# Optimization experiments

Hardware: AMD Instinct MI355X
Metric: run time of the kernel (lower is better)

## Reference

```python
import jax, jax.numpy as jnp
import numpy as np

SIZE = 64

def _init_linear(key, out_f, in_f, bias):
    k1, k2 = jax.random.split(key)
    bound = 1.0 / np.sqrt(in_f)
    W = jax.random.uniform(k1, (out_f, in_f), jnp.float32, -bound, bound)
    if bias:
        b = jax.random.uniform(k2, (out_f,), jnp.float32, -bound, bound)
        return W, b
    return W, None

def setup_inputs() -> dict:
    key = jax.random.key(0)
    ks = jax.random.split(key, 8)
    B, Lq, Lc = 16, 256, 256
    query = jax.random.normal(ks[0], (B, Lq, SIZE), jnp.float32)
    bank = jax.random.normal(ks[1], (B, Lc, SIZE), jnp.float32)
    mask = jnp.zeros((B, Lq, Lc), dtype=bool)
    Wq, _ = _init_linear(ks[2], SIZE, SIZE, False)          # linear_query (no bias)
    Wc, bc = _init_linear(ks[3], SIZE, SIZE, True)           # linear_context (bias)
    Ws, bs = _init_linear(ks[4], 1, SIZE, True)              # linear_score
    Woq, _ = _init_linear(ks[5], SIZE, SIZE, False)          # linear_out_query (no bias)
    Woc, boc = _init_linear(ks[6], SIZE, SIZE, True)         # linear_out_context (bias since mlp)
    return {"query": query, "bank": bank, "mask": mask,
            "Wq": Wq, "Wc": Wc, "bc": bc, "Ws": Ws, "bs": bs,
            "Woq": Woq, "Woc": Woc, "boc": boc}

def reference(query, bank, mask, Wq, Wc, bc, Ws, bs, Woq, Woc, boc):
    # MLP (additive) attention score: tanh(Wq q + Wc c + bc) projected to scalar
    sq = jnp.einsum('bqd,ed->bqe', query, Wq)                 # [B,Lq,D]
    sc = jnp.einsum('bcd,ed->bce', bank, Wc) + bc             # [B,Lc,D]
    h = jnp.tanh(sq[:, :, None, :] + sc[:, None, :, :])       # [B,Lq,Lc,D]
    score = jnp.einsum('bqcd,od->bqc', h, Ws) + bs[0]         # [B,Lq,Lc]
    score = jnp.where(mask, -jnp.inf, score)
    attn = jax.nn.softmax(score, axis=-1)                     # [B,Lq,Lc]
    context = jnp.einsum('bqc,bcd->bqd', attn, bank)          # [B,Lq,D]
    output = (jnp.einsum('bqd,ed->bqe', context, Woc) + boc
              + jnp.einsum('bqd,ed->bqe', query, Woq))
    return (output, attn)
```

## Files before the change

kernel.cpp:

```cpp
#include <hip/hip_runtime.h>
#include <math.h>

#define B  16
#define LQ 256
#define LC 256
#define D  64
#define QT 4
#define TS   2.88539008177793f
#define L2E  1.44269504088896f
#define PAD  72
#define INPAD 36
#define TPAD 33
#define CP4  264

__global__ __launch_bounds__(256) void proj_kernel(
    const float* __restrict__ query, const float* __restrict__ bank,
    const float* __restrict__ Wq, const float* __restrict__ Wc,
    const float* __restrict__ bc,
    const float* __restrict__ Woq, const float* __restrict__ Woc,
    const float* __restrict__ boc,
    float* __restrict__ esq, float* __restrict__ esct,
    float* __restrict__ oq, float* __restrict__ wb)
{
    int t  = threadIdx.x;
    int tp = blockIdx.x >> 7;
    int rb = blockIdx.x & 127;
    int bb_x = (rb & 7) + ((rb >> 6) << 3);
    int jj   = (rb >> 3) & 7;
    int r0 = bb_x * 256 + jj * 32;

    __shared__ __align__(16) float in_t[64 * INPAD];
    __shared__ __align__(16) float w_t [64 * PAD];
    __shared__ float tr[64 * TPAD];

    const float* src = (tp & 1) ? bank : query;
    const float* W   = (tp == 0) ? Wq : (tp == 1) ? Wc : (tp == 2) ? Woq : Woc;

    #pragma unroll
    for (int it = 0; it < 2; ++it) {
        int g = it * 256 + t;
        int kc4 = g & 15, row = g >> 4;
        float4 v = *reinterpret_cast<const float4*>(src + (r0 + row) * D + kc4 * 4);
        in_t[(kc4*4+0)*INPAD + row] = v.x; in_t[(kc4*4+1)*INPAD + row] = v.y;
        in_t[(kc4*4+2)*INPAD + row] = v.z; in_t[(kc4*4+3)*INPAD + row] = v.w;
    }
    #pragma unroll
    for (int it = 0; it < 4; ++it) {
        int g = it * 256 + t;
        int kc = (g >> 8) * 4 + (g & 3);
        int row = (g >> 2) & 63;
        float4 w = *reinterpret_cast<const float4*>(W + row * D + kc * 4);
        w_t[(kc*4+0)*PAD + row] = w.x; w_t[(kc*4+1)*PAD + row] = w.y;
        w_t[(kc*4+2)*PAD + row] = w.z; w_t[(kc*4+3)*PAD + row] = w.w;
    }
    __syncthreads();

    int cg = t & 15, rg = t >> 4;
    float acc[2][4];
    #pragma unroll
    for (int i = 0; i < 2; ++i)
        #pragma unroll
        for (int j = 0; j < 4; ++j) acc[i][j] = 0.f;

    #pragma unroll 8
    for (int k = 0; k < 64; ++k) {
        float2 a2 = *reinterpret_cast<const float2*>(&in_t[k * INPAD + rg * 2]);
        float4 w4 = *reinterpret_cast<const float4*>(&w_t [k * PAD + cg * 4]);
        acc[0][0]=fmaf(a2.x,w4.x,acc[0][0]); acc[0][1]=fmaf(a2.x,w4.y,acc[0][1]);
        acc[0][2]=fmaf(a2.x,w4.z,acc[0][2]); acc[0][3]=fmaf(a2.x,w4.w,acc[0][3]);
        acc[1][0]=fmaf(a2.y,w4.x,acc[1][0]); acc[1][1]=fmaf(a2.y,w4.y,acc[1][1]);
        acc[1][2]=fmaf(a2.y,w4.z,acc[1][2]); acc[1][3]=fmaf(a2.y,w4.w,acc[1][3]);
    }

    float4 b4 = {0.f, 0.f, 0.f, 0.f};
    if (tp == 1) b4 = *reinterpret_cast<const float4*>(bc  + cg * 4);
    if (tp == 3) b4 = *reinterpret_cast<const float4*>(boc + cg * 4);

    if (tp == 1) {
        #pragma unroll
        for (int i = 0; i < 2; ++i) {
            tr[(cg*4+0)*TPAD + rg*2+i] = exp2f(TS * (acc[i][0] + b4.x));
            tr[(cg*4+1)*TPAD + rg*2+i] = exp2f(TS * (acc[i][1] + b4.y));
            tr[(cg*4+2)*TPAD + rg*2+i] = exp2f(TS * (acc[i][2] + b4.z));
            tr[(cg*4+3)*TPAD + rg*2+i] = exp2f(TS * (acc[i][3] + b4.w));
        }
        __syncthreads();
        int bb = r0 >> 8;
        int cbase = r0 & 255;
        #pragma unroll
        for (int it = 0; it < 2; ++it) {
            int g = it * 256 + t;
            int d4 = g >> 5, cl = g & 31;
            float4 o;
            o.x = tr[(4*d4+0)*TPAD + cl];
            o.y = tr[(4*d4+1)*TPAD + cl];
            o.z = tr[(4*d4+2)*TPAD + cl];
            o.w = tr[(4*d4+3)*TPAD + cl];
            *reinterpret_cast<float4*>(esct + ((bb*16 + d4)*CP4 + cbase + cl)*4) = o;
        }
    } else {
        float* dst = (tp == 0) ? esq : (tp == 2) ? oq : wb;
        #pragma unroll
        for (int i = 0; i < 2; ++i) {
            float4 o;
            o.x = acc[i][0] + b4.x; o.y = acc[i][1] + b4.y;
            o.z = acc[i][2] + b4.z; o.w = acc[i][3] + b4.w;
            if (tp == 0) {
                o.x = exp2f(TS * o.x); o.y = exp2f(TS * o.y);
                o.z = exp2f(TS * o.z); o.w = exp2f(TS * o.w);
            }
            *reinterpret_cast<float4*>(dst + (r0 + rg*2 + i) * D + cg * 4) = o;
        }
    }
}

__global__ __launch_bounds__(256, 4) void attn_kernel(
    const unsigned char* __restrict__ mask,
    const float* __restrict__ esq_g, const float* __restrict__ esct_g,
    const float* __restrict__ Ws,
    const float* __restrict__ oq_g, const float* __restrict__ wb_g,
    float* __restrict__ out, float* __restrict__ attn_out)
{
    int t = threadIdx.x;
    int c = t;
    int p = blockIdx.x;
    int b = (p & 7) + ((p >> 9) << 3);
    int qb = (p >> 3) & 63;
    int bq0 = b * LQ + qb * QT;
    int lane = t & 63, wv = t >> 6;

    __shared__ __align__(16) float a_lds[QT][LC];
    __shared__ float part_lds[4 * QT * 64];
    __shared__ float red_s[4 * QT];

    const float* eqp = esq_g + bq0 * D;

    unsigned char mb[QT];
    #pragma unroll
    for (int qi = 0; qi < QT; ++qi) mb[qi] = mask[(bq0 + qi) * LC + c];

    const float4* ep4 = reinterpret_cast<const float4*>(esct_g) + b*16*CP4 + c;

    float s[QT];
    #pragma unroll
    for (int qi = 0; qi < QT; ++qi) s[qi] = 0.f;

    #pragma unroll
    for (int kb = 0; kb < 4; ++kb) {
        float4 ec4[4];
        #pragma unroll
        for (int j = 0; j < 4; ++j) ec4[j] = ep4[(kb*4 + j) * CP4];
        #pragma unroll
        for (int j = 0; j < 4; ++j) {
            const int d0 = kb * 16 + j * 4;
            float w0 = Ws[d0+0], w1 = Ws[d0+1];
            float w2 = Ws[d0+2], w3 = Ws[d0+3];
            #pragma unroll
            for (int qi = 0; qi < QT; ++qi) {
                float e0 = eqp[qi*D + d0+0];
                float e1 = eqp[qi*D + d0+1];
                float e2 = eqp[qi*D + d0+2];
                float e3 = eqp[qi*D + d0+3];
                float ax = fmaf(ec4[j].x, e0, 1.0f);
                float ay = fmaf(ec4[j].y, e1, 1.0f);
                float az = fmaf(ec4[j].z, e2, 1.0f);
                float aw = fmaf(ec4[j].w, e3, 1.0f);
                float pxy = ax * ay, pzw = az * aw;
                float nxy = fmaf(w0, ay, w1 * ax);
                float nzw = fmaf(w2, aw, w3 * az);
                float N   = fmaf(nxy, pzw, nzw * pxy);
                s[qi] = fmaf(N, __builtin_amdgcn_rcpf(pxy * pzw), s[qi]);
            }
        }
    }

    float a[QT];
    #pragma unroll
    for (int qi = 0; qi < QT; ++qi) {
        a[qi] = mb[qi] ? 0.0f : exp2f(-TS * s[qi]);
    }

    #pragma unroll
    for (int qi = 0; qi < QT; ++qi) a_lds[qi][c] = a[qi];
    #pragma unroll
    for (int qi = 0; qi < QT; ++qi) {
        float ss = a[qi];
        #pragma unroll
        for (int o = 32; o > 0; o >>= 1) ss += __shfl_xor(ss, o);
        if (lane == 0) red_s[wv * QT + qi] = ss;
    }
    __syncthreads();

    float rs[QT];
    #pragma unroll
    for (int qi = 0; qi < QT; ++qi) {
        float SUM = (red_s[qi] + red_s[QT + qi]) + (red_s[2*QT + qi] + red_s[3*QT + qi]);
        rs[qi] = __builtin_amdgcn_rcpf(SUM);
    }

    #pragma unroll
    for (int qi = 0; qi < QT; ++qi)
        attn_out[(bq0 + qi) * LC + c] = a[qi] * rs[qi];

    {
        int g = wv;
        float acc[QT];
        #pragma unroll
        for (int qi = 0; qi < QT; ++qi) acc[qi] = 0.f;
        const float* wbp = wb_g + (b * LC + g * 64) * D + lane;
        #pragma unroll
        for (int i0 = 0; i0 < 64; i0 += 4) {
            float4 A0 = *reinterpret_cast<const float4*>(&a_lds[0][g*64 + i0]);
            float4 A1 = *reinterpret_cast<const float4*>(&a_lds[1][g*64 + i0]);
            float4 A2 = *reinterpret_cast<const float4*>(&a_lds[2][g*64 + i0]);
            float4 A3 = *reinterpret_cast<const float4*>(&a_lds[3][g*64 + i0]);
            float w0 = wbp[(i0+0) * D];
            float w1 = wbp[(i0+1) * D];
            float w2 = wbp[(i0+2) * D];
            float w3 = wbp[(i0+3) * D];
            acc[0] = fmaf(A0.x, w0, acc[0]); acc[1] = fmaf(A1.x, w0, acc[1]);
            acc[2] = fmaf(A2.x, w0, acc[2]); acc[3] = fmaf(A3.x, w0, acc[3]);
            acc[0] = fmaf(A0.y, w1, acc[0]); acc[1] = fmaf(A1.y, w1, acc[1]);
            acc[2] = fmaf(A2.y, w1, acc[2]); acc[3] = fmaf(A3.y, w1, acc[3]);
            acc[0] = fmaf(A0.z, w2, acc[0]); acc[1] = fmaf(A1.z, w2, acc[1]);
            acc[2] = fmaf(A2.z, w2, acc[2]); acc[3] = fmaf(A3.z, w2, acc[3]);
            acc[0] = fmaf(A0.w, w3, acc[0]); acc[1] = fmaf(A1.w, w3, acc[1]);
            acc[2] = fmaf(A2.w, w3, acc[2]); acc[3] = fmaf(A3.w, w3, acc[3]);
        }
        #pragma unroll
        for (int qi = 0; qi < QT; ++qi)
            part_lds[(g * QT + qi) * 64 + lane] = acc[qi];
    }
    __syncthreads();

    {
        int qi = t >> 6, e = t & 63;
        float ps = (part_lds[(0 * QT + qi) * 64 + e] + part_lds[(1 * QT + qi) * 64 + e])
                 + (part_lds[(2 * QT + qi) * 64 + e] + part_lds[(3 * QT + qi) * 64 + e]);
        out[bq0 * D + t] = fmaf(ps, rs[qi], oq_g[bq0 * D + t]);
    }
}

extern "C" void kernel_launch(void* const* d_in, const int* in_sizes, int n_in,
                              void* d_out, int out_size, void* d_ws, size_t ws_size,
                              hipStream_t stream) {
    const float* query = (const float*)d_in[0];
    const float* bank  = (const float*)d_in[1];
    const unsigned char* mask = (const unsigned char*)d_in[2];
    const float* Wq  = (const float*)d_in[3];
    const float* Wc  = (const float*)d_in[4];
    const float* bc  = (const float*)d_in[5];
    const float* Ws  = (const float*)d_in[6];
    const float* Woq = (const float*)d_in[8];
    const float* Woc = (const float*)d_in[9];
    const float* boc = (const float*)d_in[10];

    float* out  = (float*)d_out;
    float* attn = out + B * LQ * D;

    float* esq  = (float*)d_ws;
    float* esct = esq + B * LQ * D;
    float* oq   = esct + B * 16 * CP4 * 4;
    float* wb   = oq + B * LQ * D;

    proj_kernel<<<4 * 128, 256, 0, stream>>>(query, bank, Wq, Wc, bc,
                                             Woq, Woc, boc,
                                             esq, esct, oq, wb);
    attn_kernel<<<B * LQ / QT, 256, 0, stream>>>(mask, esq, esct, Ws,
                                                 oq, wb, out, attn);
}
```

Measured before the change: 22.56 us.

## Fuse query-side projections into attention kernel, halve projection grid

```diff
diff --git a/kernel.cpp b/kernel.cpp
--- a/kernel.cpp
+++ b/kernel.cpp
@@ -13,17 +13,14 @@
 #define TPAD 33
 #define CP4  264
 
-__global__ __launch_bounds__(256) void proj_kernel(
-    const float* __restrict__ query, const float* __restrict__ bank,
-    const float* __restrict__ Wq, const float* __restrict__ Wc,
-    const float* __restrict__ bc,
-    const float* __restrict__ Woq, const float* __restrict__ Woc,
-    const float* __restrict__ boc,
-    float* __restrict__ esq, float* __restrict__ esct,
-    float* __restrict__ oq, float* __restrict__ wb)
+__global__ __launch_bounds__(256) void bank_proj_kernel(
+    const float* __restrict__ bank,
+    const float* __restrict__ Wc, const float* __restrict__ bc,
+    const float* __restrict__ Woc, const float* __restrict__ boc,
+    float* __restrict__ esct, float* __restrict__ wb)
 {
     int t  = threadIdx.x;
-    int tp = blockIdx.x >> 7;
+    int tp1 = (blockIdx.x >> 7) == 0;
     int rb = blockIdx.x & 127;
     int bb_x = (rb & 7) + ((rb >> 6) << 3);
     int jj   = (rb >> 3) & 7;
@@ -33,14 +30,13 @@
     __shared__ __align__(16) float w_t [64 * PAD];
     __shared__ float tr[64 * TPAD];
 
-    const float* src = (tp & 1) ? bank : query;
-    const float* W   = (tp == 0) ? Wq : (tp == 1) ? Wc : (tp == 2) ? Woq : Woc;
+    const float* W = tp1 ? Wc : Woc;
 
     #pragma unroll
     for (int it = 0; it < 2; ++it) {
         int g = it * 256 + t;
         int kc4 = g & 15, row = g >> 4;
-        float4 v = *reinterpret_cast<const float4*>(src + (r0 + row) * D + kc4 * 4);
+        float4 v = *reinterpret_cast<const float4*>(bank + (r0 + row) * D + kc4 * 4);
         in_t[(kc4*4+0)*INPAD + row] = v.x; in_t[(kc4*4+1)*INPAD + row] = v.y;
         in_t[(kc4*4+2)*INPAD + row] = v.z; in_t[(kc4*4+3)*INPAD + row] = v.w;
     }
@@ -72,11 +68,10 @@
         acc[1][2]=fmaf(a2.y,w4.z,acc[1][2]); acc[1][3]=fmaf(a2.y,w4.w,acc[1][3]);
     }
 
-    float4 b4 = {0.f, 0.f, 0.f, 0.f};
-    if (tp == 1) b4 = *reinterpret_cast<const float4*>(bc  + cg * 4);
-    if (tp == 3) b4 = *reinterpret_cast<const float4*>(boc + cg * 4);
-
-    if (tp == 1) {
+    float4 b4 = tp1 ? *reinterpret_cast<const float4*>(bc  + cg * 4)
+                    : *reinterpret_cast<const float4*>(boc + cg * 4);
+
+    if (tp1) {
         #pragma unroll
         for (int i = 0; i < 2; ++i) {
             tr[(cg*4+0)*TPAD + rg*2+i] = exp2f(TS * (acc[i][0] + b4.x));
@@ -99,26 +94,22 @@
             *reinterpret_cast<float4*>(esct + ((bb*16 + d4)*CP4 + cbase + cl)*4) = o;
         }
     } else {
-        float* dst = (tp == 0) ? esq : (tp == 2) ? oq : wb;
         #pragma unroll
         for (int i = 0; i < 2; ++i) {
             float4 o;
             o.x = acc[i][0] + b4.x; o.y = acc[i][1] + b4.y;
             o.z = acc[i][2] + b4.z; o.w = acc[i][3] + b4.w;
-            if (tp == 0) {
-                o.x = exp2f(TS * o.x); o.y = exp2f(TS * o.y);
-                o.z = exp2f(TS * o.z); o.w = exp2f(TS * o.w);
-            }
-            *reinterpret_cast<float4*>(dst + (r0 + rg*2 + i) * D + cg * 4) = o;
+            *reinterpret_cast<float4*>(wb + (r0 + rg*2 + i) * D + cg * 4) = o;
         }
     }
 }
 
 __global__ __launch_bounds__(256, 4) void attn_kernel(
+    const float* __restrict__ query,
     const unsigned char* __restrict__ mask,
-    const float* __restrict__ esq_g, const float* __restrict__ esct_g,
-    const float* __restrict__ Ws,
-    const float* __restrict__ oq_g, const float* __restrict__ wb_g,
+    const float* __restrict__ Wq, const float* __restrict__ Woq,
+    const float* __restrict__ esct_g, const float* __restrict__ Ws,
+    const float* __restrict__ wb_g,
     float* __restrict__ out, float* __restrict__ attn_out)
 {
     int t = threadIdx.x;
@@ -129,15 +120,33 @@
     int bq0 = b * LQ + qb * QT;
     int lane = t & 63, wv = t >> 6;
 
+    __shared__ __align__(16) float esq_lds[QT][D];
     __shared__ __align__(16) float a_lds[QT][LC];
     __shared__ float part_lds[4 * QT * 64];
     __shared__ float red_s[4 * QT];
 
-    const float* eqp = esq_g + bq0 * D;
+    int qi0 = __builtin_amdgcn_readfirstlane(wv);
+    const float* qp  = query + (bq0 + qi0) * D;
+    const float* wqr = Wq  + lane * D;
+    const float* wor = Woq + lane * D;
+    float sq = 0.f, oqv = 0.f;
+    #pragma unroll
+    for (int kc = 0; kc < 16; ++kc) {
+        float4 wq4 = *reinterpret_cast<const float4*>(wqr + kc * 4);
+        float4 wo4 = *reinterpret_cast<const float4*>(wor + kc * 4);
+        float q0 = qp[kc*4+0], q1 = qp[kc*4+1], q2 = qp[kc*4+2], q3 = qp[kc*4+3];
+        sq  = fmaf(wq4.x, q0, sq);  sq  = fmaf(wq4.y, q1, sq);
+        sq  = fmaf(wq4.z, q2, sq);  sq  = fmaf(wq4.w, q3, sq);
+        oqv = fmaf(wo4.x, q0, oqv); oqv = fmaf(wo4.y, q1, oqv);
+        oqv = fmaf(wo4.z, q2, oqv); oqv = fmaf(wo4.w, q3, oqv);
+    }
+    esq_lds[qi0][lane] = exp2f(TS * sq);
 
     unsigned char mb[QT];
     #pragma unroll
     for (int qi = 0; qi < QT; ++qi) mb[qi] = mask[(bq0 + qi) * LC + c];
+
+    __syncthreads();
 
     const float4* ep4 = reinterpret_cast<const float4*>(esct_g) + b*16*CP4 + c;
 
@@ -157,14 +166,11 @@
             float w2 = Ws[d0+2], w3 = Ws[d0+3];
             #pragma unroll
             for (int qi = 0; qi < QT; ++qi) {
-                float e0 = eqp[qi*D + d0+0];
-                float e1 = eqp[qi*D + d0+1];
-                float e2 = eqp[qi*D + d0+2];
-                float e3 = eqp[qi*D + d0+3];
-                float ax = fmaf(ec4[j].x, e0, 1.0f);
-                float ay = fmaf(ec4[j].y, e1, 1.0f);
-                float az = fmaf(ec4[j].z, e2, 1.0f);
-                float aw = fmaf(ec4[j].w, e3, 1.0f);
+                float4 e4 = *reinterpret_cast<const float4*>(&esq_lds[qi][d0]);
+                float ax = fmaf(ec4[j].x, e4.x, 1.0f);
+                float ay = fmaf(ec4[j].y, e4.y, 1.0f);
+                float az = fmaf(ec4[j].z, e4.z, 1.0f);
+                float aw = fmaf(ec4[j].w, e4.w, 1.0f);
                 float pxy = ax * ay, pzw = az * aw;
                 float nxy = fmaf(w0, ay, w1 * ax);
                 float nzw = fmaf(w2, aw, w3 * az);
@@ -237,7 +243,7 @@
         int qi = t >> 6, e = t & 63;
         float ps = (part_lds[(0 * QT + qi) * 64 + e] + part_lds[(1 * QT + qi) * 64 + e])
                  + (part_lds[(2 * QT + qi) * 64 + e] + part_lds[(3 * QT + qi) * 64 + e]);
-        out[bq0 * D + t] = fmaf(ps, rs[qi], oq_g[bq0 * D + t]);
+        out[bq0 * D + t] = fmaf(ps, rs[qi], oqv);
     }
 }
 
@@ -258,14 +264,10 @@
     float* out  = (float*)d_out;
     float* attn = out + B * LQ * D;
 
-    float* esq  = (float*)d_ws;
-    float* esct = esq + B * LQ * D;
-    float* oq   = esct + B * 16 * CP4 * 4;
-    float* wb   = oq + B * LQ * D;
-
-    proj_kernel<<<4 * 128, 256, 0, stream>>>(query, bank, Wq, Wc, bc,
-                                             Woq, Woc, boc,
-                                             esq, esct, oq, wb);
-    attn_kernel<<<B * LQ / QT, 256, 0, stream>>>(mask, esq, esct, Ws,
-                                                 oq, wb, out, attn);
+    float* esct = (float*)d_ws;
+    float* wb   = esct + B * 16 * CP4 * 4;
+
+    bank_proj_kernel<<<256, 256, 0, stream>>>(bank, Wc, bc, Woc, boc, esct, wb);
+    attn_kernel<<<B * LQ / QT, 256, 0, stream>>>(query, mask, Wq, Woq, esct, Ws,
+                                                 wb, out, attn);
 }
```

Result: slower. 34.46 us (+52.7%).
